# Kernel tuning notes

Measured on AMD Instinct MI355X. Metric: run time of the kernel, lower is better.

Reference implementation:

```python
import jax, jax.numpy as jnp
import numpy as np


def setup_inputs() -> dict:
    key = jax.random.key(0)
    k1, k2, k3, k4, k5 = jax.random.split(key, 5)
    d_in, d_out, r = 1024, 1024, 32
    x = jax.random.normal(k1, (8, 8192, d_in), dtype=jnp.float32)
    W = jax.random.normal(k2, (d_out, d_in), dtype=jnp.float32) * (1.0 / np.sqrt(d_in))
    b = jax.random.normal(k3, (d_out,), dtype=jnp.float32) * 0.01
    V_r = jax.random.normal(k4, (d_in, r), dtype=jnp.float32) * (1.0 / np.sqrt(d_in))
    C = jax.random.normal(k5, (d_out, r), dtype=jnp.float32) * (1.0 / np.sqrt(r))
    return {"x": x, "W": W, "b": b, "V_r": V_r, "C": C}


def reference(x, W, b, V_r, C):
    # base = x @ W.T + b  (the quantized linear, modeled in fp32)
    base = jnp.einsum('bsd,od->bso', x, W) + b
    # low-rank correction: (x @ V_r) @ C.T  -- keep factored form, never
    # materialize the dense d_in x d_out correction matrix
    correction = jnp.einsum('bsr,or->bso', jnp.einsum('bsd,dr->bsr', x, V_r), C)
    return base + correction
```

## Files before the change

kernel.cpp:

```cpp
#include <hip/hip_runtime.h>
#include <hip/hip_bf16.h>

typedef __bf16 bf16_t;
typedef __bf16 bf16x8 __attribute__((ext_vector_type(8)));
typedef float  f32x4  __attribute__((ext_vector_type(4)));

#define DK 1024
#define DN 1024
#define RNK 32
#define BM 128
#define BN 512
#define BK 32
#define NKT 32

__global__ void weff_kernel(const float* __restrict__ W,
                            const float* __restrict__ Vr,
                            const float* __restrict__ C,
                            bf16_t* __restrict__ WeffSw)
{
    const int o  = blockIdx.x;
    const int g  = threadIdx.x;
    const int d0 = g * 8;

    f32x4 cv[8];
#pragma unroll
    for (int q = 0; q < 8; ++q) cv[q] = *(const f32x4*)(C + o * RNK + q * 4);

    const f32x4* wrow = (const f32x4*)(W + (size_t)o * DK + d0);
    f32x4 w0 = wrow[0], w1 = wrow[1];
    float acc[8];
#pragma unroll
    for (int e = 0; e < 4; ++e) { acc[e] = w0[e]; acc[4 + e] = w1[e]; }

#pragma unroll
    for (int e = 0; e < 8; ++e) {
        const f32x4* vre = (const f32x4*)(Vr + (size_t)(d0 + e) * RNK);
        float s = 0.f;
#pragma unroll
        for (int q = 0; q < 8; ++q) {
            f32x4 v = vre[q];
            s += cv[q][0] * v[0] + cv[q][1] * v[1] + cv[q][2] * v[2] + cv[q][3] * v[3];
        }
        acc[e] += s;
    }

    bf16x8 out;
#pragma unroll
    for (int e = 0; e < 8; ++e) out[e] = (bf16_t)acc[e];

    const int bn = o >> 9, rloc = o & 511;
    const int kt = d0 >> 5, seg = (d0 >> 3) & 3;
    const int sw = seg ^ ((rloc >> 1) & 3);
    const size_t byte = (size_t)(bn * 32 + kt) * 32768 + rloc * 64 + (sw << 4);
    *(bf16x8*)((char*)WeffSw + byte) = out;
}

__global__ __launch_bounds__(512, 1) void corrlin_gemm_kernel(
    const float* __restrict__ X, const bf16_t* __restrict__ WeffSw,
    const float* __restrict__ bias, float* __restrict__ Out)
{
    __shared__ __align__(16) char smem[81920];
    char* Ab0 = smem;
    char* Ab1 = smem + 8192;
    char* Bb0 = smem + 16384;
    char* Bb1 = smem + 49152;

    const int tid = threadIdx.x;
    const int b0  = blockIdx.x;
    const int L  = (b0 & 7) * 128 + (b0 >> 3);
    const int bm = L >> 1;
    const int bn = L & 1;
    const int m0 = bm * BM;

    const int lane = tid & 63;
    const int wn   = tid >> 6;
    const int arow = tid >> 2;
    const int aseg = tid & 3;

    f32x4 acc[8][4] = {};
    f32x4 set0[2], set1[2];

    auto issueA = [&](int kt, f32x4* s) {
        const float* p = X + (size_t)(m0 + arow) * DK + kt * BK + aseg * 8;
        s[0] = *(const f32x4*)p;
        s[1] = *(const f32x4*)(p + 4);
    };
    auto storeA = [&](const f32x4* s, char* Ab) {
        const int sw = aseg ^ ((arow >> 1) & 3);
        bf16x8 v;
#pragma unroll
        for (int j = 0; j < 4; ++j) { v[j] = (bf16_t)s[0][j]; v[4 + j] = (bf16_t)s[1][j]; }
        *(bf16x8*)(Ab + arow * 64 + (sw << 4)) = v;
    };
    auto issueB = [&](int kt, char* Bb) {
        const char* g = (const char*)WeffSw + (size_t)(bn * 32 + kt) * 32768;
#pragma unroll
        for (int c = 0; c < 4; ++c) {
            const int lin = c * 8192 + wn * 1024;
            __builtin_amdgcn_global_load_lds(
                (const __attribute__((address_space(1))) void*)(g + lin + lane * 16),
                (__attribute__((address_space(3))) void*)(Bb + lin),
                16, 0, 0);
        }
    };
    auto readB = [&](const char* Bc, bf16x8* bfr) {
        const int kb = lane >> 4;
#pragma unroll
        for (int nf = 0; nf < 4; ++nf) {
            const int row = wn * 64 + nf * 16 + (lane & 15);
            bfr[nf] = *(const bf16x8*)(Bc + row * 64 + ((kb ^ ((row >> 1) & 3)) << 4));
        }
    };
    auto compute_h = [&](const char* Ac, int h, const bf16x8* bfr) {
        bf16x8 af[4];
        const int kb = lane >> 4;
#pragma unroll
        for (int i = 0; i < 4; ++i) {
            const int row = (h * 4 + i) * 16 + (lane & 15);
            af[i] = *(const bf16x8*)(Ac + row * 64 + ((kb ^ ((row >> 1) & 3)) << 4));
        }
        __builtin_amdgcn_s_setprio(1);
#pragma unroll
        for (int i = 0; i < 4; ++i)
#pragma unroll
            for (int nf = 0; nf < 4; ++nf)
                acc[h * 4 + i][nf] = __builtin_amdgcn_mfma_f32_16x16x32_bf16(
                    af[i], bfr[nf], acc[h * 4 + i][nf], 0, 0, 0);
        __builtin_amdgcn_s_setprio(0);
    };

    auto iter = [&](int t, const char* Ac, const char* Bc, char* An, char* Bn,
                    f32x4* aStore , f32x4* aFill ) {
        if (t + 1 < NKT) issueB(t + 1, Bn);
        bf16x8 bfr[4];
        readB(Bc, bfr);
        compute_h(Ac, 0, bfr);
        if (t + 1 < NKT) storeA(aStore, An);
        if (t + 2 < NKT) issueA(t + 2, aFill);
        compute_h(Ac, 1, bfr);
        if (t + 2 < NKT) {
            asm volatile("s_waitcnt vmcnt(2) lgkmcnt(0)" ::: "memory");
            __builtin_amdgcn_s_barrier();
        } else if (t + 1 < NKT) {
            asm volatile("s_waitcnt vmcnt(0) lgkmcnt(0)" ::: "memory");
            __builtin_amdgcn_s_barrier();
        }
    };

    issueA(0, set0);
    issueB(0, Bb0);
    storeA(set0, Ab0);
    issueA(1, set1);
    asm volatile("s_waitcnt vmcnt(2) lgkmcnt(0)" ::: "memory");
    __builtin_amdgcn_s_barrier();

    for (int t = 0; t < NKT; t += 2) {
        iter(t,     Ab0, Bb0, Ab1, Bb1, set1, set0);
        iter(t + 1, Ab1, Bb1, Ab0, Bb0, set0, set1);
    }
    __syncthreads();

    float* tb = (float*)smem + wn * 1280;
    const int nbase = bn * BN + wn * 64;
    float bv[4];
#pragma unroll
    for (int nf = 0; nf < 4; ++nf) bv[nf] = bias[nbase + nf * 16 + (lane & 15)];

#pragma unroll
    for (int mf = 0; mf < 8; ++mf) {
#pragma unroll
        for (int nf = 0; nf < 4; ++nf)
#pragma unroll
            for (int j = 0; j < 4; ++j) {
                const int r = (lane >> 4) * 4 + j;
                const int c = nf * 16 + (lane & 15);
                tb[r * 80 + c] = acc[mf][nf][j] + bv[nf];
            }
        __syncthreads();
#pragma unroll
        for (int jj = 0; jj < 4; ++jj) {
            const int rr = jj * 4 + (lane >> 4);
            const int cc = (lane & 15) * 4;
            f32x4 v = *(const f32x4*)&tb[rr * 80 + cc];
            *(f32x4*)&Out[(size_t)(m0 + mf * 16 + rr) * DN + nbase + cc] = v;
        }
        __syncthreads();
    }
}

extern "C" void kernel_launch(void* const* d_in, const int* in_sizes, int n_in,
                              void* d_out, int out_size, void* d_ws, size_t ws_size,
                              hipStream_t stream) {
    const float* x  = (const float*)d_in[0];
    const float* W  = (const float*)d_in[1];
    const float* b  = (const float*)d_in[2];
    const float* Vr = (const float*)d_in[3];
    const float* C  = (const float*)d_in[4];
    float* out = (float*)d_out;

    const int M = in_sizes[0] / DK;
    bf16_t* WeffSw = (bf16_t*)d_ws;

    weff_kernel<<<DN, 128, 0, stream>>>(W, Vr, C, WeffSw);

    const int mtiles = M / BM;
    const int nwg = mtiles * (DN / BN);
    corrlin_gemm_kernel<<<nwg, 512, 0, stream>>>(x, WeffSw, b, out);
}
```

Measured before the change: 204.3 us.

## Double K tile depth and single-buffer B via register prefetch

Raises the K tile from 32 to 64, halving the number of k-iterations and barriers. Weff gets a new swizzled layout with 128-byte rows. B is now single-buffered in LDS: each wave reads all its B fragments into registers, hits a barrier, and only then issues the next global-to-LDS B load, which frees LDS for a larger A double buffer. Launch bounds request two blocks per CU, but 96KB of LDS per block and the added registers make that occupancy uncertain, and the extra barrier per iteration may serialize the B load against compute.

```diff
diff --git a/kernel.cpp b/kernel.cpp
--- a/kernel.cpp
+++ b/kernel.cpp
@@ -10,8 +10,8 @@
 #define RNK 32
 #define BM 128
 #define BN 512
-#define BK 32
-#define NKT 32
+#define BK 64
+#define NKT 16
 
 __global__ void weff_kernel(const float* __restrict__ W,
                             const float* __restrict__ Vr,
@@ -49,21 +49,20 @@
     for (int e = 0; e < 8; ++e) out[e] = (bf16_t)acc[e];
 
     const int bn = o >> 9, rloc = o & 511;
-    const int kt = d0 >> 5, seg = (d0 >> 3) & 3;
-    const int sw = seg ^ ((rloc >> 1) & 3);
-    const size_t byte = (size_t)(bn * 32 + kt) * 32768 + rloc * 64 + (sw << 4);
+    const int kt = g >> 3, kgrp = g & 7;
+    const size_t byte = (size_t)(bn * 16 + kt) * 65536
+                      + rloc * 128 + ((kgrp * 16) ^ ((rloc & 7) << 4));
     *(bf16x8*)((char*)WeffSw + byte) = out;
 }
 
-__global__ __launch_bounds__(512, 1) void corrlin_gemm_kernel(
+__global__ __launch_bounds__(512, 2) void corrlin_gemm_kernel(
     const float* __restrict__ X, const bf16_t* __restrict__ WeffSw,
     const float* __restrict__ bias, float* __restrict__ Out)
 {
-    __shared__ __align__(16) char smem[81920];
-    char* Ab0 = smem;
-    char* Ab1 = smem + 8192;
-    char* Bb0 = smem + 16384;
-    char* Bb1 = smem + 49152;
+    __shared__ __align__(16) char smem[98304];
+    char* Ab0  = smem;
+    char* Ab1  = smem + 16384;
+    char* Blds = smem + 32768;
 
     const int tid = threadIdx.x;
     const int b0  = blockIdx.x;
@@ -73,51 +72,57 @@
     const int m0 = bm * BM;
 
     const int lane = tid & 63;
-    const int wn   = tid >> 6;
+    const int wid  = tid >> 6;
     const int arow = tid >> 2;
     const int aseg = tid & 3;
 
     f32x4 acc[8][4] = {};
-    f32x4 set0[2], set1[2];
+    f32x4 set0[4], set1[4];
 
     auto issueA = [&](int kt, f32x4* s) {
-        const float* p = X + (size_t)(m0 + arow) * DK + kt * BK + aseg * 8;
-        s[0] = *(const f32x4*)p;
-        s[1] = *(const f32x4*)(p + 4);
+        const float* p = X + (size_t)(m0 + arow) * DK + kt * BK + aseg * 16;
+#pragma unroll
+        for (int j = 0; j < 4; ++j) s[j] = *(const f32x4*)(p + j * 4);
     };
     auto storeA = [&](const f32x4* s, char* Ab) {
-        const int sw = aseg ^ ((arow >> 1) & 3);
-        bf16x8 v;
-#pragma unroll
-        for (int j = 0; j < 4; ++j) { v[j] = (bf16_t)s[0][j]; v[4 + j] = (bf16_t)s[1][j]; }
-        *(bf16x8*)(Ab + arow * 64 + (sw << 4)) = v;
-    };
-    auto issueB = [&](int kt, char* Bb) {
-        const char* g = (const char*)WeffSw + (size_t)(bn * 32 + kt) * 32768;
-#pragma unroll
-        for (int c = 0; c < 4; ++c) {
-            const int lin = c * 8192 + wn * 1024;
+        const int rsw = (arow & 7) << 4;
+#pragma unroll
+        for (int j = 0; j < 2; ++j) {
+            bf16x8 v;
+#pragma unroll
+            for (int e = 0; e < 4; ++e) { v[e] = (bf16_t)s[j * 2][e]; v[4 + e] = (bf16_t)s[j * 2 + 1][e]; }
+            const int kgrp = aseg * 2 + j;
+            *(bf16x8*)(Ab + arow * 128 + ((kgrp * 16) ^ rsw)) = v;
+        }
+    };
+    auto issueB = [&](int kt) {
+        const char* g = (const char*)WeffSw + (size_t)(bn * 16 + kt) * 65536;
+#pragma unroll
+        for (int c = 0; c < 8; ++c) {
+            const int lin = wid * 8192 + c * 1024;
             __builtin_amdgcn_global_load_lds(
                 (const __attribute__((address_space(1))) void*)(g + lin + lane * 16),
-                (__attribute__((address_space(3))) void*)(Bb + lin),
+                (__attribute__((address_space(3))) void*)(Blds + lin),
                 16, 0, 0);
         }
     };
-    auto readB = [&](const char* Bc, bf16x8* bfr) {
-        const int kb = lane >> 4;
-#pragma unroll
-        for (int nf = 0; nf < 4; ++nf) {
-            const int row = wn * 64 + nf * 16 + (lane & 15);
-            bfr[nf] = *(const bf16x8*)(Bc + row * 64 + ((kb ^ ((row >> 1) & 3)) << 4));
-        }
-    };
-    auto compute_h = [&](const char* Ac, int h, const bf16x8* bfr) {
+    auto readBall = [&](bf16x8* bfr) {
+#pragma unroll
+        for (int ks = 0; ks < 2; ++ks)
+#pragma unroll
+            for (int nf = 0; nf < 4; ++nf) {
+                const int row = wid * 64 + nf * 16 + (lane & 15);
+                const int kb  = ks * 64 + (lane >> 4) * 16;
+                bfr[ks * 4 + nf] = *(const bf16x8*)(Blds + row * 128 + (kb ^ ((row & 7) << 4)));
+            }
+    };
+    auto computeH = [&](const char* Ac, int ks, int h, const bf16x8* bfr) {
         bf16x8 af[4];
-        const int kb = lane >> 4;
+        const int kb = ks * 64 + (lane >> 4) * 16;
 #pragma unroll
         for (int i = 0; i < 4; ++i) {
             const int row = (h * 4 + i) * 16 + (lane & 15);
-            af[i] = *(const bf16x8*)(Ac + row * 64 + ((kb ^ ((row >> 1) & 3)) << 4));
+            af[i] = *(const bf16x8*)(Ac + row * 128 + (kb ^ ((row & 7) << 4)));
         }
         __builtin_amdgcn_s_setprio(1);
 #pragma unroll
@@ -129,17 +134,21 @@
         __builtin_amdgcn_s_setprio(0);
     };
 
-    auto iter = [&](int t, const char* Ac, const char* Bc, char* An, char* Bn,
+    auto iter = [&](int t, const char* Ac, char* An,
                     f32x4* aStore , f32x4* aFill ) {
-        if (t + 1 < NKT) issueB(t + 1, Bn);
-        bf16x8 bfr[4];
-        readB(Bc, bfr);
-        compute_h(Ac, 0, bfr);
+        bf16x8 bfr[8];
+        readBall(bfr);
+        asm volatile("s_waitcnt lgkmcnt(0)" ::: "memory");
+        __builtin_amdgcn_s_barrier();
+        if (t + 1 < NKT) issueB(t + 1);
+        computeH(Ac, 0, 0, bfr);
+        computeH(Ac, 0, 1, bfr);
         if (t + 1 < NKT) storeA(aStore, An);
         if (t + 2 < NKT) issueA(t + 2, aFill);
-        compute_h(Ac, 1, bfr);
+        computeH(Ac, 1, 0, bfr + 4);
+        computeH(Ac, 1, 1, bfr + 4);
         if (t + 2 < NKT) {
-            asm volatile("s_waitcnt vmcnt(2) lgkmcnt(0)" ::: "memory");
+            asm volatile("s_waitcnt vmcnt(4) lgkmcnt(0)" ::: "memory");
             __builtin_amdgcn_s_barrier();
         } else if (t + 1 < NKT) {
             asm volatile("s_waitcnt vmcnt(0) lgkmcnt(0)" ::: "memory");
@@ -148,20 +157,20 @@
     };
 
     issueA(0, set0);
-    issueB(0, Bb0);
+    issueB(0);
     storeA(set0, Ab0);
     issueA(1, set1);
-    asm volatile("s_waitcnt vmcnt(2) lgkmcnt(0)" ::: "memory");
+    asm volatile("s_waitcnt vmcnt(4) lgkmcnt(0)" ::: "memory");
     __builtin_amdgcn_s_barrier();
 
     for (int t = 0; t < NKT; t += 2) {
-        iter(t,     Ab0, Bb0, Ab1, Bb1, set1, set0);
-        iter(t + 1, Ab1, Bb1, Ab0, Bb0, set0, set1);
+        iter(t,     Ab0, Ab1, set1, set0);
+        iter(t + 1, Ab1, Ab0, set0, set1);
     }
     __syncthreads();
 
-    float* tb = (float*)smem + wn * 1280;
-    const int nbase = bn * BN + wn * 64;
+    float* tb = (float*)smem + wid * 1280;
+    const int nbase = bn * BN + wid * 64;
     float bv[4];
 #pragma unroll
     for (int nf = 0; nf < 4; ++nf) bv[nf] = bias[nbase + nf * 16 + (lane & 15)];
```

Measured after the change: 372.8 us. 82.5% more time.

## Deepen GEMM prefetch pipeline to four B stages and register-staged A tiles

Applied to the files above, without the earlier changes.

Extends the software pipeline from double buffering to a deeper prefetch. B tiles move to a 4-slot LDS ring loaded 3 iterations ahead, and A is held in four register sets loaded 4 iterations ahead, with a higher vmcnt threshold so more global loads stay in flight. The goal is to hide global memory latency for the streamed fp32 X and the bf16 weights. In exchange it uses 144KB of LDS, plus extra registers for the A staging sets, and needs a peeled tail with a full drain.

```diff
diff --git a/kernel.cpp b/kernel.cpp
--- a/kernel.cpp
+++ b/kernel.cpp
@@ -59,11 +59,13 @@
     const float* __restrict__ X, const bf16_t* __restrict__ WeffSw,
     const float* __restrict__ bias, float* __restrict__ Out)
 {
-    __shared__ __align__(16) char smem[81920];
+    __shared__ __align__(16) char smem[147456];
     char* Ab0 = smem;
     char* Ab1 = smem + 8192;
-    char* Bb0 = smem + 16384;
-    char* Bb1 = smem + 49152;
+    char* Bq0 = smem + 16384;
+    char* Bq1 = smem + 49152;
+    char* Bq2 = smem + 81920;
+    char* Bq3 = smem + 114688;
 
     const int tid = threadIdx.x;
     const int b0  = blockIdx.x;
@@ -78,7 +80,7 @@
     const int aseg = tid & 3;
 
     f32x4 acc[8][4] = {};
-    f32x4 set0[2], set1[2];
+    f32x4 s0[2], s1[2], s2[2], s3[2];
 
     auto issueA = [&](int kt, f32x4* s) {
         const float* p = X + (size_t)(m0 + arow) * DK + kt * BK + aseg * 8;
@@ -129,35 +131,59 @@
         __builtin_amdgcn_s_setprio(0);
     };
 
-    auto iter = [&](int t, const char* Ac, const char* Bc, char* An, char* Bn,
-                    f32x4* aStore , f32x4* aFill ) {
-        if (t + 1 < NKT) issueB(t + 1, Bn);
+    auto iter_main = [&](int t, const char* Ac, char* An, const char* Bc, char* Bn3,
+                         const f32x4* sStore , f32x4* sFill ) {
+        issueB(t + 3, Bn3);
         bf16x8 bfr[4];
         readB(Bc, bfr);
         compute_h(Ac, 0, bfr);
-        if (t + 1 < NKT) storeA(aStore, An);
-        if (t + 2 < NKT) issueA(t + 2, aFill);
+        storeA(sStore, An);
+        issueA(t + 4, sFill);
         compute_h(Ac, 1, bfr);
-        if (t + 2 < NKT) {
-            asm volatile("s_waitcnt vmcnt(2) lgkmcnt(0)" ::: "memory");
-            __builtin_amdgcn_s_barrier();
-        } else if (t + 1 < NKT) {
+        asm volatile("s_waitcnt vmcnt(14) lgkmcnt(0)" ::: "memory");
+        __builtin_amdgcn_s_barrier();
+    };
+    auto iter_tail = [&](int t, const char* Ac, char* An, const char* Bc, char* Bn3,
+                         const f32x4* sStore, f32x4* sFill) {
+        if (t + 3 < NKT) issueB(t + 3, Bn3);
+        bf16x8 bfr[4];
+        readB(Bc, bfr);
+        compute_h(Ac, 0, bfr);
+        if (t + 1 < NKT) storeA(sStore, An);
+        if (t + 4 < NKT) issueA(t + 4, sFill);
+        compute_h(Ac, 1, bfr);
+        if (t + 1 < NKT) {
             asm volatile("s_waitcnt vmcnt(0) lgkmcnt(0)" ::: "memory");
             __builtin_amdgcn_s_barrier();
         }
     };
 
-    issueA(0, set0);
-    issueB(0, Bb0);
-    storeA(set0, Ab0);
-    issueA(1, set1);
-    asm volatile("s_waitcnt vmcnt(2) lgkmcnt(0)" ::: "memory");
+    issueA(0, s0);
+    issueB(0, Bq0);
+    storeA(s0, Ab0);
+    issueA(1, s1);
+    asm volatile("s_waitcnt vmcnt(0)" ::: "memory");
+    issueB(1, Bq1);
+    issueA(2, s2);
+    issueB(2, Bq2);
+    issueA(3, s3);
+    asm volatile("s_waitcnt lgkmcnt(0)" ::: "memory");
     __builtin_amdgcn_s_barrier();
 
-    for (int t = 0; t < NKT; t += 2) {
-        iter(t,     Ab0, Bb0, Ab1, Bb1, set1, set0);
-        iter(t + 1, Ab1, Bb1, Ab0, Bb0, set0, set1);
+    for (int t = 0; t < 24; t += 4) {
+        iter_main(t,     Ab0, Ab1, Bq0, Bq3, s1, s0);
+        iter_main(t + 1, Ab1, Ab0, Bq1, Bq0, s2, s1);
+        iter_main(t + 2, Ab0, Ab1, Bq2, Bq1, s3, s2);
+        iter_main(t + 3, Ab1, Ab0, Bq3, Bq2, s0, s3);
     }
+    iter_tail(24, Ab0, Ab1, Bq0, Bq3, s1, s0);
+    iter_tail(25, Ab1, Ab0, Bq1, Bq0, s2, s1);
+    iter_tail(26, Ab0, Ab1, Bq2, Bq1, s3, s2);
+    iter_tail(27, Ab1, Ab0, Bq3, Bq2, s0, s3);
+    iter_tail(28, Ab0, Ab1, Bq0, Bq3, s1, s0);
+    iter_tail(29, Ab1, Ab0, Bq1, Bq0, s2, s1);
+    iter_tail(30, Ab0, Ab1, Bq2, Bq1, s3, s2);
+    iter_tail(31, Ab1, Ab0, Bq3, Bq2, s0, s3);
     __syncthreads();
 
     float* tb = (float*)smem + wn * 1280;
```

Result: no change. 202.7 us (-0.8%).

## Load X tiles via direct global-to-LDS DMA with triple-buffered pipeline

Applied to the files above, without the earlier changes.

The A operand (fp32 X) now goes straight into LDS through global_load_lds instead of being staged in registers, converted to bf16 and stored by the threads. The bf16 conversion moves to the fragment read in compute. The pipeline changes from double to triple buffering, with loads issued two k-tiles ahead and a fixed vmcnt wait. LDS use rises to 144KB because A is stored as fp32, and each fragment read now needs two 16-byte LDS loads plus conversion ALU work in the inner loop.

```diff
diff --git a/kernel.cpp b/kernel.cpp
--- a/kernel.cpp
+++ b/kernel.cpp
@@ -55,15 +55,17 @@
     *(bf16x8*)((char*)WeffSw + byte) = out;
 }
 
-__global__ __launch_bounds__(512, 1) void corrlin_gemm_kernel(
+__global__ __launch_bounds__(512, 1) void corrlin_gemm_dma(
     const float* __restrict__ X, const bf16_t* __restrict__ WeffSw,
     const float* __restrict__ bias, float* __restrict__ Out)
 {
-    __shared__ __align__(16) char smem[81920];
-    char* Ab0 = smem;
-    char* Ab1 = smem + 8192;
-    char* Bb0 = smem + 16384;
-    char* Bb1 = smem + 49152;
+    __shared__ __align__(16) char smem[147456];
+    char* Aq0 = smem;
+    char* Aq1 = smem + 16384;
+    char* Aq2 = smem + 32768;
+    char* Bq0 = smem + 49152;
+    char* Bq1 = smem + 81920;
+    char* Bq2 = smem + 114688;
 
     const int tid = threadIdx.x;
     const int b0  = blockIdx.x;
@@ -74,23 +76,21 @@
 
     const int lane = tid & 63;
     const int wn   = tid >> 6;
-    const int arow = tid >> 2;
-    const int aseg = tid & 3;
 
     f32x4 acc[8][4] = {};
-    f32x4 set0[2], set1[2];
-
-    auto issueA = [&](int kt, f32x4* s) {
-        const float* p = X + (size_t)(m0 + arow) * DK + kt * BK + aseg * 8;
-        s[0] = *(const f32x4*)p;
-        s[1] = *(const f32x4*)(p + 4);
-    };
-    auto storeA = [&](const f32x4* s, char* Ab) {
-        const int sw = aseg ^ ((arow >> 1) & 3);
-        bf16x8 v;
-#pragma unroll
-        for (int j = 0; j < 4; ++j) { v[j] = (bf16_t)s[0][j]; v[4 + j] = (bf16_t)s[1][j]; }
-        *(bf16x8*)(Ab + arow * 64 + (sw << 4)) = v;
+
+    auto issueA = [&](int kt, char* Ab) {
+#pragma unroll
+        for (int c = 0; c < 2; ++c) {
+            const int g16 = wn * 128 + c * 64 + lane;
+            const int row = g16 >> 3;
+            const int half = (g16 & 7) ^ (row & 7);
+            const float* src = X + (size_t)(m0 + row) * DK + kt * 32 + half * 4;
+            __builtin_amdgcn_global_load_lds(
+                (const __attribute__((address_space(1))) void*)src,
+                (__attribute__((address_space(3))) void*)(Ab + wn * 2048 + c * 1024),
+                16, 0, 0);
+        }
     };
     auto issueB = [&](int kt, char* Bb) {
         const char* g = (const char*)WeffSw + (size_t)(bn * 32 + kt) * 32768;
@@ -117,7 +117,11 @@
 #pragma unroll
         for (int i = 0; i < 4; ++i) {
             const int row = (h * 4 + i) * 16 + (lane & 15);
-            af[i] = *(const bf16x8*)(Ac + row * 64 + ((kb ^ ((row >> 1) & 3)) << 4));
+            const int rs = row & 7;
+            f32x4 v0 = *(const f32x4*)(Ac + row * 128 + (((kb * 2)     ^ rs) << 4));
+            f32x4 v1 = *(const f32x4*)(Ac + row * 128 + (((kb * 2 + 1) ^ rs) << 4));
+#pragma unroll
+            for (int j = 0; j < 4; ++j) { af[i][j] = (bf16_t)v0[j]; af[i][4 + j] = (bf16_t)v1[j]; }
         }
         __builtin_amdgcn_s_setprio(1);
 #pragma unroll
@@ -129,34 +133,40 @@
         __builtin_amdgcn_s_setprio(0);
     };
 
-    auto iter = [&](int t, const char* Ac, const char* Bc, char* An, char* Bn,
-                    f32x4* aStore , f32x4* aFill ) {
-        if (t + 1 < NKT) issueB(t + 1, Bn);
+    auto iterM = [&](int t, const char* Ac, const char* Bc, char* An2, char* Bn2) {
+        issueB(t + 2, Bn2);
+        issueA(t + 2, An2);
         bf16x8 bfr[4];
         readB(Bc, bfr);
         compute_h(Ac, 0, bfr);
-        if (t + 1 < NKT) storeA(aStore, An);
-        if (t + 2 < NKT) issueA(t + 2, aFill);
         compute_h(Ac, 1, bfr);
-        if (t + 2 < NKT) {
-            asm volatile("s_waitcnt vmcnt(2) lgkmcnt(0)" ::: "memory");
-            __builtin_amdgcn_s_barrier();
-        } else if (t + 1 < NKT) {
-            asm volatile("s_waitcnt vmcnt(0) lgkmcnt(0)" ::: "memory");
-            __builtin_amdgcn_s_barrier();
-        }
-    };
-
-    issueA(0, set0);
-    issueB(0, Bb0);
-    storeA(set0, Ab0);
-    issueA(1, set1);
-    asm volatile("s_waitcnt vmcnt(2) lgkmcnt(0)" ::: "memory");
+        asm volatile("s_waitcnt vmcnt(6) lgkmcnt(0)" ::: "memory");
+        __builtin_amdgcn_s_barrier();
+    };
+
+    issueB(0, Bq0); issueA(0, Aq0);
+    issueB(1, Bq1); issueA(1, Aq1);
+    asm volatile("s_waitcnt vmcnt(6)" ::: "memory");
     __builtin_amdgcn_s_barrier();
 
-    for (int t = 0; t < NKT; t += 2) {
-        iter(t,     Ab0, Bb0, Ab1, Bb1, set1, set0);
-        iter(t + 1, Ab1, Bb1, Ab0, Bb0, set0, set1);
+    for (int t = 0; t < 30; t += 3) {
+        iterM(t,     Aq0, Bq0, Aq2, Bq2);
+        iterM(t + 1, Aq1, Bq1, Aq0, Bq0);
+        iterM(t + 2, Aq2, Bq2, Aq1, Bq1);
+    }
+    {
+        bf16x8 bfr[4];
+        readB(Bq0, bfr);
+        compute_h(Aq0, 0, bfr);
+        compute_h(Aq0, 1, bfr);
+        asm volatile("s_waitcnt vmcnt(0) lgkmcnt(0)" ::: "memory");
+        __builtin_amdgcn_s_barrier();
+    }
+    {
+        bf16x8 bfr[4];
+        readB(Bq1, bfr);
+        compute_h(Aq1, 0, bfr);
+        compute_h(Aq1, 1, bfr);
     }
     __syncthreads();
 
@@ -205,5 +215,5 @@
 
     const int mtiles = M / BM;
     const int nwg = mtiles * (DN / BN);
-    corrlin_gemm_kernel<<<nwg, 512, 0, stream>>>(x, WeffSw, b, out);
+    corrlin_gemm_dma<<<nwg, 512, 0, stream>>>(x, WeffSw, b, out);
 }
```

New measurement: 208.6 us. +2.1%, slower.
